# Performance work log

Measured on AMD Instinct MI355X. Metric: run time of the kernel, lower is better.

Reference implementation:

```python
import jax, jax.numpy as jnp
import numpy as np

HEADS = 4
TOKEN_DIM = 128
SCALE = (TOKEN_DIM // HEADS) ** -0.5


def _conv1x1(x, w, b):
    # x: (B,C,D,H,W), w: (O,C), b: (O,)
    return jnp.einsum('bcdhw,oc->bodhw', x, w) + b[None, :, None, None, None]


def _flatten(x):
    # (B,C,D,H,W) -> (B,L,C)
    B, C = x.shape[0], x.shape[1]
    return x.reshape(B, C, -1).transpose(0, 2, 1)


def _mha(q, k, v):
    # q: (B,Lq,D), k/v: (B,Lk,D)
    B, Lq, Dq = q.shape
    Lk = k.shape[1]
    hd = Dq // HEADS
    qh = q.reshape(B, Lq, HEADS, hd).transpose(0, 2, 1, 3)
    kh = k.reshape(B, Lk, HEADS, hd).transpose(0, 2, 1, 3)
    vh = v.reshape(B, Lk, HEADS, hd).transpose(0, 2, 1, 3)
    attn = jnp.einsum('bhqd,bhkd->bhqk', qh, kh) * SCALE
    attn = jax.nn.softmax(attn, axis=-1)
    out = jnp.einsum('bhqk,bhkd->bhqd', attn, vh)
    return out.transpose(0, 2, 1, 3).reshape(B, Lq, Dq)


def setup_inputs() -> dict:
    key = jax.random.key(0)
    ks = jax.random.split(key, 10)
    B, C, D, H, W = 2, 64, 16, 16, 16
    return {
        'feat_ct': jax.random.normal(ks[0], (B, C, D, H, W), jnp.float32),
        'feat_pet': jax.random.normal(ks[1], (B, C, D, H, W), jnp.float32),
        'wq': jax.random.normal(ks[2], (TOKEN_DIM, C), jnp.float32) * 0.05,
        'bq': jax.random.normal(ks[3], (TOKEN_DIM,), jnp.float32) * 0.05,
        'wk': jax.random.normal(ks[4], (TOKEN_DIM, C), jnp.float32) * 0.05,
        'bk': jax.random.normal(ks[5], (TOKEN_DIM,), jnp.float32) * 0.05,
        'wv': jax.random.normal(ks[6], (TOKEN_DIM, C), jnp.float32) * 0.05,
        'bv': jax.random.normal(ks[7], (TOKEN_DIM,), jnp.float32) * 0.05,
        'wo': jax.random.normal(ks[8], (C, TOKEN_DIM), jnp.float32) * 0.05,
        'bo': jax.random.normal(ks[9], (C,), jnp.float32) * 0.05,
    }


def reference(feat_ct, feat_pet, wq, bq, wk, bk, wv, bv, wo, bo):
    B, C, D, H, W = feat_ct.shape
    q_ct = _flatten(_conv1x1(feat_ct, wq, bq))
    k_ct = _flatten(_conv1x1(feat_ct, wk, bk))
    v_ct = _flatten(_conv1x1(feat_ct, wv, bv))
    q_pet = _flatten(_conv1x1(feat_pet, wq, bq))
    k_pet = _flatten(_conv1x1(feat_pet, wk, bk))
    v_pet = _flatten(_conv1x1(feat_pet, wv, bv))

    ct_attn = _mha(q_ct, k_pet, v_pet)
    pet_attn = _mha(q_pet, k_ct, v_ct)

    # Original torch code does view(B, token_dim, -1).permute(0,2,1) followed by
    # unflatten's permute(0,2,1) -> net effect is a raw reinterpretation of the
    # contiguous (B, L, token_dim) buffer as (B, token_dim, D, H, W): a reshape.
    fused_ct = ((ct_attn + q_ct) * 0.5).reshape(B, TOKEN_DIM, D, H, W)
    fused_ct = _conv1x1(fused_ct, wo, bo)  # dropout is identity (eval)
    fused_pet = ((pet_attn + q_pet) * 0.5).reshape(B, TOKEN_DIM, D, H, W)
    fused_pet = _conv1x1(fused_pet, wo, bo)

    return feat_ct + fused_ct, feat_pet + fused_pet
```

## Files before the change

kernel.cpp:

```cpp
#include <hip/hip_runtime.h>

typedef __bf16 bf16x8 __attribute__((ext_vector_type(8)));
typedef float f32x4 __attribute__((ext_vector_type(4)));
typedef float f32x16 __attribute__((ext_vector_type(16)));
typedef unsigned short u16x8 __attribute__((ext_vector_type(8)));
typedef unsigned int u32x4 __attribute__((ext_vector_type(4)));
typedef unsigned int u32x2 __attribute__((ext_vector_type(2)));

constexpr int C_ = 64, TD_ = 128, L_ = 4096, B_ = 2, H_ = 4, HD_ = 32;
constexpr float SCALE_LOG2E = 0.25504821365f;

#if __has_builtin(__builtin_amdgcn_exp2f)
#define EXP2F __builtin_amdgcn_exp2f
#else
#define EXP2F exp2f
#endif

static __device__ __forceinline__ unsigned short f2bf(float f) {
  unsigned u = __builtin_bit_cast(unsigned, f);
  u += 0x7fffu + ((u >> 16) & 1u);
  return (unsigned short)(u >> 16);
}
static __device__ __forceinline__ float bf2f(unsigned short h) {
  unsigned u = ((unsigned)h) << 16;
  return __builtin_bit_cast(float, u);
}
static __device__ __forceinline__ unsigned cvt_pk_bf16(float lo, float hi) {
  unsigned r;
  asm("v_cvt_pk_bf16_f32 %0, %1, %2" : "=v"(r) : "v"(lo), "v"(hi));
  return r;
}
static __device__ __forceinline__ void plane_swap(unsigned& a, unsigned& b) {
  asm("v_permlane32_swap_b32 %0, %1" : "+v"(a), "+v"(b));
}
static __device__ __forceinline__ float xhalf_add(float x) {
  float a = x, b = x;
  asm("v_permlane32_swap_b32 %0, %1" : "+v"(a), "+v"(b));
  return a + b;
}
static __device__ __forceinline__ int rowf(int r, int hi) {
  return (r & 3) + 8 * (r >> 2) + 4 * hi;
}
static __device__ __forceinline__ bf16x8 pack8(const float* v) {
  unsigned p0 = cvt_pk_bf16(v[0], v[1]);
  unsigned p1 = cvt_pk_bf16(v[2], v[3]);
  unsigned p2 = cvt_pk_bf16(v[4], v[5]);
  unsigned p3 = cvt_pk_bf16(v[6], v[7]);
  return __builtin_bit_cast(bf16x8, (u32x4){p0, p1, p2, p3});
}

__global__ __launch_bounds__(256) void proj_kernel(
    const float* __restrict__ fct, const float* __restrict__ fpet,
    const float* __restrict__ wq, const float* __restrict__ bq,
    const float* __restrict__ wk, const float* __restrict__ bk,
    const float* __restrict__ wv, const float* __restrict__ bv,
    unsigned short* __restrict__ Qbf, unsigned short* __restrict__ Kbf,
    unsigned short* __restrict__ Vt, float* __restrict__ QT)
{
  __shared__ __align__(16) unsigned short Tb[2][32][136];

  int bid = blockIdx.x;
  int lt = bid & 127, mb = bid >> 7;
  int l0 = lt * 32;
  int b = mb & 1;
  const float* xb = (mb >= 2 ? fpet : fct) + (size_t)b * C_ * L_;

  int lane = threadIdx.x & 63, wid = threadIdx.x >> 6;
  int l31 = lane & 31, hi = lane >> 5;
  int o0 = wid * 96;

  bf16x8 Bf[4];
  #pragma unroll
  for (int ch = 0; ch < 4; ++ch) {
    float v[8];
    #pragma unroll
    for (int j = 0; j < 8; ++j)
      v[j] = xb[(size_t)(ch * 16 + hi * 8 + j) * L_ + l0 + l31];
    Bf[ch] = pack8(v);
  }

  const f32x16 Z = {0.f, 0.f, 0.f, 0.f, 0.f, 0.f, 0.f, 0.f,
                    0.f, 0.f, 0.f, 0.f, 0.f, 0.f, 0.f, 0.f};
  f32x16 acc[3] = {Z, Z, Z};

  #pragma unroll
  for (int t = 0; t < 3; ++t) {
    int oa = o0 + t * 32;
    int which = oa >> 7, od = oa & 127;
    const float* W = which == 0 ? wq : (which == 1 ? wk : wv);
    #pragma unroll
    for (int ch = 0; ch < 4; ++ch) {
      const float* wr = W + (size_t)(od + l31) * C_ + ch * 16 + hi * 8;
      float a[8];
      #pragma unroll
      for (int j = 0; j < 8; ++j) a[j] = wr[j];
      bf16x8 Af = pack8(a);
      acc[t] = __builtin_amdgcn_mfma_f32_32x32x16_bf16(Af, Bf[ch], acc[t], 0, 0, 0);
    }
  }

  #pragma unroll
  for (int t = 0; t < 3; ++t) {
    int oa = o0 + t * 32;
    int which = oa >> 7, od = oa & 127;
    const float* Bs = which == 0 ? bq : (which == 1 ? bk : bv);
    if (which == 2) {
      #pragma unroll
      for (int r = 0; r < 16; ++r) {
        int o = od + rowf(r, hi);
        Vt[((size_t)mb * TD_ + o) * L_ + l0 + l31] = f2bf(acc[t][r] + Bs[o]);
      }
    } else {
      if (which == 0) {
        #pragma unroll
        for (int r = 0; r < 16; ++r) {
          int o = od + rowf(r, hi);
          QT[((size_t)mb * TD_ + o) * L_ + l0 + l31] = acc[t][r] + Bs[o];
        }
      }
      float sc = which == 0 ? SCALE_LOG2E : 1.0f;
      #pragma unroll
      for (int rg = 0; rg < 4; ++rg) {
        int cb = od + 8 * rg + 4 * hi;
        float y0 = (acc[t][rg * 4 + 0] + Bs[cb + 0]) * sc;
        float y1 = (acc[t][rg * 4 + 1] + Bs[cb + 1]) * sc;
        float y2 = (acc[t][rg * 4 + 2] + Bs[cb + 2]) * sc;
        float y3 = (acc[t][rg * 4 + 3] + Bs[cb + 3]) * sc;
        u32x2 pk = {cvt_pk_bf16(y0, y1), cvt_pk_bf16(y2, y3)};
        *(u32x2*)&Tb[which][l31][cb] = pk;
      }
    }
  }
  __syncthreads();

  int lrd = threadIdx.x & 31, sel = threadIdx.x >> 5;
  #pragma unroll
  for (int bufi = 0; bufi < 2; ++bufi) {
    unsigned short* dstg = bufi ? Kbf : Qbf;
    #pragma unroll
    for (int it = 0; it < 2; ++it) {
      int idx = it * 8 + sel;
      int h = idx >> 2, dc = idx & 3;
      u16x8 v = *(const u16x8*)&Tb[bufi][lrd][h * 32 + dc * 8];
      *(u16x8*)&dstg[(((size_t)mb * H_ + h) * L_ + l0 + lrd) * HD_ + dc * 8] = v;
    }
  }
}

static __device__ __forceinline__ void softmax_pv(
    const f32x16& S, float& lp, f32x16& O, bf16x8 vc0, bf16x8 vc1)
{
  float p[16];
  #pragma unroll
  for (int i = 0; i < 16; ++i) p[i] = EXP2F(S[i]);
  float s0 = (p[0] + p[1]) + (p[2] + p[3]);
  float s1 = (p[4] + p[5]) + (p[6] + p[7]);
  float s2 = (p[8] + p[9]) + (p[10] + p[11]);
  float s3 = (p[12] + p[13]) + (p[14] + p[15]);
  lp += (s0 + s1) + (s2 + s3);

  unsigned w0 = cvt_pk_bf16(p[0], p[1]);
  unsigned w1 = cvt_pk_bf16(p[2], p[3]);
  unsigned w2 = cvt_pk_bf16(p[4], p[5]);
  unsigned w3 = cvt_pk_bf16(p[6], p[7]);
  unsigned w4 = cvt_pk_bf16(p[8], p[9]);
  unsigned w5 = cvt_pk_bf16(p[10], p[11]);
  unsigned w6 = cvt_pk_bf16(p[12], p[13]);
  unsigned w7 = cvt_pk_bf16(p[14], p[15]);
  plane_swap(w0, w2);
  plane_swap(w1, w3);
  plane_swap(w4, w6);
  plane_swap(w5, w7);
  bf16x8 pf0 = __builtin_bit_cast(bf16x8, (u32x4){w0, w1, w2, w3});
  bf16x8 pf1 = __builtin_bit_cast(bf16x8, (u32x4){w4, w5, w6, w7});

  O = __builtin_amdgcn_mfma_f32_32x32x16_bf16(vc0, pf0, O, 0, 0, 0);
  O = __builtin_amdgcn_mfma_f32_32x32x16_bf16(vc1, pf1, O, 0, 0, 0);
}

__global__ __launch_bounds__(256, 4) void attn_kernel(
    const unsigned short* __restrict__ Qbf, const unsigned short* __restrict__ Kbf,
    const unsigned short* __restrict__ Vt, const float* __restrict__ QT,
    float* __restrict__ Fused)
{
  __shared__ __align__(16) float Obuf[4][64][33];
  __shared__ float lbuf[4][64];

  int bid = blockIdx.x;
  int x = bid & 7, local = bid >> 3;
  int g = 2 * x + (local & 1);
  int qg = local >> 1;
  int h = g & 3, b = (g >> 2) & 1, dir = g >> 3;

  int lane = threadIdx.x & 63, wid = threadIdx.x >> 6;
  int l31 = lane & 31, hi = lane >> 5;
  int q0 = qg * 64;
  int qmb = dir * B_ + b, kmb = (1 - dir) * B_ + b;
  int k0 = wid * 1024;

  const unsigned short* qbase = Qbf + (size_t)(qmb * H_ + h) * L_ * HD_;
  bf16x8 qb[2][2];
  #pragma unroll
  for (int s = 0; s < 2; ++s)
    #pragma unroll
    for (int c = 0; c < 2; ++c)
      qb[s][c] = *(const bf16x8*)(qbase + (q0 + s * 32 + l31) * HD_ + c * 16 + hi * 8);

  const unsigned short* kp =
      Kbf + (size_t)(kmb * H_ + h) * L_ * HD_ + (k0 + l31) * HD_ + hi * 8;
  const unsigned short* vp =
      Vt + (size_t)(kmb * TD_ + h * HD_ + l31) * L_ + k0 + hi * 8;

  const f32x16 Z = {0.f, 0.f, 0.f, 0.f, 0.f, 0.f, 0.f, 0.f,
                    0.f, 0.f, 0.f, 0.f, 0.f, 0.f, 0.f, 0.f};
  f32x16 Oa[2] = {Z, Z};
  float lp[2] = {0.f, 0.f};

  bf16x8 kc0 = *(const bf16x8*)(kp);
  bf16x8 kc1 = *(const bf16x8*)(kp + 16);
  bf16x8 vc0 = *(const bf16x8*)(vp);
  bf16x8 vc1 = *(const bf16x8*)(vp + 16);

  #pragma unroll 4
  for (int t = 0; t < 32; ++t) {
    bf16x8 kn0 = *(const bf16x8*)(kp + (t + 1) * 1024);
    bf16x8 kn1 = *(const bf16x8*)(kp + (t + 1) * 1024 + 16);
    bf16x8 vn0 = *(const bf16x8*)(vp + (t + 1) * 32);
    bf16x8 vn1 = *(const bf16x8*)(vp + (t + 1) * 32 + 16);
    #pragma unroll
    for (int s = 0; s < 2; ++s) {
      f32x16 S = __builtin_amdgcn_mfma_f32_32x32x16_bf16(kc0, qb[s][0], Z, 0, 0, 0);
      S = __builtin_amdgcn_mfma_f32_32x32x16_bf16(kc1, qb[s][1], S, 0, 0, 0);
      softmax_pv(S, lp[s], Oa[s], vc0, vc1);
    }
    kc0 = kn0; kc1 = kn1; vc0 = vn0; vc1 = vn1;
  }

  lp[0] = xhalf_add(lp[0]);
  lp[1] = xhalf_add(lp[1]);
  if (hi == 0) {
    lbuf[wid][l31] = lp[0];
    lbuf[wid][32 + l31] = lp[1];
  }
  #pragma unroll
  for (int r = 0; r < 16; ++r) {
    int d = rowf(r, hi);
    Obuf[wid][l31][d] = Oa[0][r];
    Obuf[wid][32 + l31][d] = Oa[1][r];
  }
  __syncthreads();

  float T = (lbuf[0][lane] + lbuf[1][lane]) + (lbuf[2][lane] + lbuf[3][lane]);
  float inv = 1.0f / T;
  const float* qtp = QT + ((size_t)qmb * TD_ + h * HD_) * L_ + q0 + lane;
  float vals[8];
  #pragma unroll
  for (int j = 0; j < 8; ++j) {
    int d = wid * 8 + j;
    float acc = (Obuf[0][lane][d] + Obuf[1][lane][d]) +
                (Obuf[2][lane][d] + Obuf[3][lane][d]);
    vals[j] = (acc * inv + qtp[(size_t)d * L_]) * 0.5f;
  }
  __syncthreads();
  #pragma unroll
  for (int j = 0; j < 8; ++j) Obuf[0][lane][wid * 8 + j] = vals[j];
  __syncthreads();
  int q = threadIdx.x >> 2, dq = threadIdx.x & 3;
  f32x4 u0 = *(const f32x4*)&Obuf[0][q][dq * 8];
  f32x4 u1 = *(const f32x4*)&Obuf[0][q][dq * 8 + 4];
  float* dst = Fused + ((size_t)qmb * L_ + q0 + q) * TD_ + h * HD_ + dq * 8;
  *(f32x4*)dst = u0;
  *(f32x4*)(dst + 4) = u1;
}

__global__ __launch_bounds__(256) void epi_kernel(
    const float* __restrict__ fct, const float* __restrict__ fpet,
    const float* __restrict__ wo, const float* __restrict__ bo,
    const float* __restrict__ Fused, float* __restrict__ out)
{
  __shared__ __align__(16) float red[2][32][33];

  int bid = blockIdx.x;
  int lt = bid & 127, im = bid >> 7;
  int b = im & 1, d = im >> 1;
  int l0 = lt * 32;
  int lr = l0 >> 7, col0 = l0 & 127;

  int lane = threadIdx.x & 63, wid = threadIdx.x >> 6;
  int l31 = lane & 31, hi = lane >> 5;
  int mt = wid & 1, kh = wid >> 1;
  int c0 = mt * 32;

  const float* Fb = Fused + (size_t)im * L_ * TD_;
  const f32x16 Z = {0.f, 0.f, 0.f, 0.f, 0.f, 0.f, 0.f, 0.f,
                    0.f, 0.f, 0.f, 0.f, 0.f, 0.f, 0.f, 0.f};
  f32x16 acc = Z;

  #pragma unroll
  for (int ch = 0; ch < 4; ++ch) {
    int cha = kh * 4 + ch;
    const float* wr = wo + (size_t)(c0 + l31) * TD_ + cha * 16 + hi * 8;
    float ah[8], al[8], vh[8], vl[8];
    #pragma unroll
    for (int j = 0; j < 8; ++j) {
      float v = wr[j];
      float hf = bf2f(f2bf(v));
      ah[j] = hf;
      al[j] = v - hf;
    }
    #pragma unroll
    for (int j = 0; j < 8; ++j) {
      int o = cha * 16 + hi * 8 + j;
      float v = Fb[(size_t)(o * 32 + lr) * TD_ + col0 + l31];
      float hf = bf2f(f2bf(v));
      vh[j] = hf;
      vl[j] = v - hf;
    }
    bf16x8 Ah = pack8(ah), Al = pack8(al);
    bf16x8 Bh = pack8(vh), Bl = pack8(vl);
    acc = __builtin_amdgcn_mfma_f32_32x32x16_bf16(Ah, Bh, acc, 0, 0, 0);
    acc = __builtin_amdgcn_mfma_f32_32x32x16_bf16(Ah, Bl, acc, 0, 0, 0);
    acc = __builtin_amdgcn_mfma_f32_32x32x16_bf16(Al, Bh, acc, 0, 0, 0);
  }

  if (kh == 1) {
    #pragma unroll
    for (int r = 0; r < 16; ++r) red[mt][rowf(r, hi)][l31] = acc[r];
  }
  __syncthreads();
  if (kh == 0) {
    const float* feat = (d ? fpet : fct) + (size_t)b * C_ * L_;
    float* ob = out + (size_t)im * C_ * L_;
    int l = l0 + l31;
    #pragma unroll
    for (int r = 0; r < 16; ++r) {
      int row = rowf(r, hi);
      int c = c0 + row;
      float v = acc[r] + red[mt][row][l31];
      ob[(size_t)c * L_ + l] = feat[(size_t)c * L_ + l] + bo[c] + v;
    }
  }
}

extern "C" void kernel_launch(void* const* d_in, const int* in_sizes, int n_in,
                              void* d_out, int out_size, void* d_ws, size_t ws_size,
                              hipStream_t stream)
{
  const float* fct  = (const float*)d_in[0];
  const float* fpet = (const float*)d_in[1];
  const float* wq = (const float*)d_in[2];
  const float* bq = (const float*)d_in[3];
  const float* wk = (const float*)d_in[4];
  const float* bk = (const float*)d_in[5];
  const float* wv = (const float*)d_in[6];
  const float* bv = (const float*)d_in[7];
  const float* wo = (const float*)d_in[8];
  const float* bo = (const float*)d_in[9];
  float* out = (float*)d_out;

  unsigned short* Qbf = (unsigned short*)d_ws;
  unsigned short* Kbf = Qbf + 2097152;
  unsigned short* Vt  = Kbf + 2097152;
  float* QT    = (float*)(Vt + 2097152);
  float* Fused = QT + 2097152;

  proj_kernel<<<512, 256, 0, stream>>>(fct, fpet, wq, bq, wk, bk, wv, bv,
                                       Qbf, Kbf, Vt, QT);
  attn_kernel<<<1024, 256, 0, stream>>>(Qbf, Kbf, Vt, QT, Fused);
  epi_kernel<<<512, 256, 0, stream>>>(fct, fpet, wo, bo, Fused, out);
}
```

Measured before the change: 158.1 us.

## Split projection grid by Q/K/V, store fused output as bf16 hi/lo pairs

The projection kernel now launches three times as many blocks, each computing one of Q, K or V for a 32-token tile, so each block does less work and more blocks run in parallel. The attention epilogue packs its partial outputs as fp16 in shared memory and writes the fused result as two bf16 planes (high and low) instead of fp32. The output kernel then loads those planes with vector reads, transposes them through shared memory, and feeds them straight to the split-precision MFMA without converting on the fly. The cross-wave reduction in fp16 and the bf16 hi+lo representation may lose a little precision, and the extra projection blocks reload the input features three times.

```diff
diff --git a/kernel.cpp b/kernel.cpp
--- a/kernel.cpp
+++ b/kernel.cpp
@@ -3,6 +3,7 @@
 typedef __bf16 bf16x8 __attribute__((ext_vector_type(8)));
 typedef float f32x4 __attribute__((ext_vector_type(4)));
 typedef float f32x16 __attribute__((ext_vector_type(16)));
+typedef _Float16 f16x2 __attribute__((ext_vector_type(2)));
 typedef unsigned short u16x8 __attribute__((ext_vector_type(8)));
 typedef unsigned int u32x4 __attribute__((ext_vector_type(4)));
 typedef unsigned int u32x2 __attribute__((ext_vector_type(2)));
@@ -29,6 +30,9 @@
   unsigned r;
   asm("v_cvt_pk_bf16_f32 %0, %1, %2" : "=v"(r) : "v"(lo), "v"(hi));
   return r;
+}
+static __device__ __forceinline__ unsigned cvt_pk_f16(float lo, float hi) {
+  return __builtin_bit_cast(unsigned, __builtin_amdgcn_cvt_pkrtz(lo, hi));
 }
 static __device__ __forceinline__ void plane_swap(unsigned& a, unsigned& b) {
   asm("v_permlane32_swap_b32 %0, %1" : "+v"(a), "+v"(b));
@@ -57,93 +61,73 @@
     unsigned short* __restrict__ Qbf, unsigned short* __restrict__ Kbf,
     unsigned short* __restrict__ Vt, float* __restrict__ QT)
 {
-  __shared__ __align__(16) unsigned short Tb[2][32][136];
+  __shared__ __align__(16) unsigned short Tb[32][136];
 
   int bid = blockIdx.x;
-  int lt = bid & 127, mb = bid >> 7;
+  int lt = bid & 127;
+  int rest = bid >> 7;
+  int mb = rest & 3;
+  int which = rest >> 2;
   int l0 = lt * 32;
   int b = mb & 1;
   const float* xb = (mb >= 2 ? fpet : fct) + (size_t)b * C_ * L_;
 
   int lane = threadIdx.x & 63, wid = threadIdx.x >> 6;
   int l31 = lane & 31, hi = lane >> 5;
-  int o0 = wid * 96;
-
-  bf16x8 Bf[4];
+  int od = wid * 32;
+
+  const float* W  = which == 0 ? wq : (which == 1 ? wk : wv);
+  const float* Bs = which == 0 ? bq : (which == 1 ? bk : bv);
+
+  const f32x16 Z = {0.f, 0.f, 0.f, 0.f, 0.f, 0.f, 0.f, 0.f,
+                    0.f, 0.f, 0.f, 0.f, 0.f, 0.f, 0.f, 0.f};
+  f32x16 acc = Z;
   #pragma unroll
   for (int ch = 0; ch < 4; ++ch) {
-    float v[8];
+    float v[8], a[8];
     #pragma unroll
     for (int j = 0; j < 8; ++j)
       v[j] = xb[(size_t)(ch * 16 + hi * 8 + j) * L_ + l0 + l31];
-    Bf[ch] = pack8(v);
-  }
-
-  const f32x16 Z = {0.f, 0.f, 0.f, 0.f, 0.f, 0.f, 0.f, 0.f,
-                    0.f, 0.f, 0.f, 0.f, 0.f, 0.f, 0.f, 0.f};
-  f32x16 acc[3] = {Z, Z, Z};
-
-  #pragma unroll
-  for (int t = 0; t < 3; ++t) {
-    int oa = o0 + t * 32;
-    int which = oa >> 7, od = oa & 127;
-    const float* W = which == 0 ? wq : (which == 1 ? wk : wv);
-    #pragma unroll
-    for (int ch = 0; ch < 4; ++ch) {
-      const float* wr = W + (size_t)(od + l31) * C_ + ch * 16 + hi * 8;
-      float a[8];
-      #pragma unroll
-      for (int j = 0; j < 8; ++j) a[j] = wr[j];
-      bf16x8 Af = pack8(a);
-      acc[t] = __builtin_amdgcn_mfma_f32_32x32x16_bf16(Af, Bf[ch], acc[t], 0, 0, 0);
-    }
-  }
-
-  #pragma unroll
-  for (int t = 0; t < 3; ++t) {
-    int oa = o0 + t * 32;
-    int which = oa >> 7, od = oa & 127;
-    const float* Bs = which == 0 ? bq : (which == 1 ? bk : bv);
-    if (which == 2) {
+    const float* wr = W + (size_t)(od + l31) * C_ + ch * 16 + hi * 8;
+    #pragma unroll
+    for (int j = 0; j < 8; ++j) a[j] = wr[j];
+    acc = __builtin_amdgcn_mfma_f32_32x32x16_bf16(pack8(a), pack8(v), acc, 0, 0, 0);
+  }
+
+  if (which == 2) {
+    #pragma unroll
+    for (int r = 0; r < 16; ++r) {
+      int o = od + rowf(r, hi);
+      Vt[((size_t)mb * TD_ + o) * L_ + l0 + l31] = f2bf(acc[r] + Bs[o]);
+    }
+  } else {
+    if (which == 0) {
       #pragma unroll
       for (int r = 0; r < 16; ++r) {
         int o = od + rowf(r, hi);
-        Vt[((size_t)mb * TD_ + o) * L_ + l0 + l31] = f2bf(acc[t][r] + Bs[o]);
+        QT[((size_t)mb * TD_ + o) * L_ + l0 + l31] = acc[r] + Bs[o];
       }
-    } else {
-      if (which == 0) {
-        #pragma unroll
-        for (int r = 0; r < 16; ++r) {
-          int o = od + rowf(r, hi);
-          QT[((size_t)mb * TD_ + o) * L_ + l0 + l31] = acc[t][r] + Bs[o];
-        }
-      }
-      float sc = which == 0 ? SCALE_LOG2E : 1.0f;
-      #pragma unroll
-      for (int rg = 0; rg < 4; ++rg) {
-        int cb = od + 8 * rg + 4 * hi;
-        float y0 = (acc[t][rg * 4 + 0] + Bs[cb + 0]) * sc;
-        float y1 = (acc[t][rg * 4 + 1] + Bs[cb + 1]) * sc;
-        float y2 = (acc[t][rg * 4 + 2] + Bs[cb + 2]) * sc;
-        float y3 = (acc[t][rg * 4 + 3] + Bs[cb + 3]) * sc;
-        u32x2 pk = {cvt_pk_bf16(y0, y1), cvt_pk_bf16(y2, y3)};
-        *(u32x2*)&Tb[which][l31][cb] = pk;
-      }
-    }
-  }
-  __syncthreads();
-
-  int lrd = threadIdx.x & 31, sel = threadIdx.x >> 5;
-  #pragma unroll
-  for (int bufi = 0; bufi < 2; ++bufi) {
-    unsigned short* dstg = bufi ? Kbf : Qbf;
-    #pragma unroll
-    for (int it = 0; it < 2; ++it) {
-      int idx = it * 8 + sel;
-      int h = idx >> 2, dc = idx & 3;
-      u16x8 v = *(const u16x8*)&Tb[bufi][lrd][h * 32 + dc * 8];
-      *(u16x8*)&dstg[(((size_t)mb * H_ + h) * L_ + l0 + lrd) * HD_ + dc * 8] = v;
-    }
+    }
+    float sc = which == 0 ? SCALE_LOG2E : 1.0f;
+    #pragma unroll
+    for (int rg = 0; rg < 4; ++rg) {
+      int cb = od + 8 * rg + 4 * hi;
+      float y0 = (acc[rg * 4 + 0] + Bs[cb + 0]) * sc;
+      float y1 = (acc[rg * 4 + 1] + Bs[cb + 1]) * sc;
+      float y2 = (acc[rg * 4 + 2] + Bs[cb + 2]) * sc;
+      float y3 = (acc[rg * 4 + 3] + Bs[cb + 3]) * sc;
+      u32x2 pk = {cvt_pk_bf16(y0, y1), cvt_pk_bf16(y2, y3)};
+      *(u32x2*)&Tb[l31][cb] = pk;
+    }
+    __syncthreads();
+    unsigned short* dstg = which ? Kbf : Qbf;
+    int row = threadIdx.x >> 3, chunk = threadIdx.x & 7;
+    int h = chunk >> 1, d0 = (chunk & 1) * 16;
+    u16x8 v0 = *(const u16x8*)&Tb[row][chunk * 16];
+    u16x8 v1 = *(const u16x8*)&Tb[row][chunk * 16 + 8];
+    size_t gb = (((size_t)mb * H_ + h) * L_ + l0 + row) * HD_ + d0;
+    *(u16x8*)&dstg[gb] = v0;
+    *(u16x8*)&dstg[gb + 8] = v1;
   }
 }
 
@@ -181,9 +165,9 @@
 __global__ __launch_bounds__(256, 4) void attn_kernel(
     const unsigned short* __restrict__ Qbf, const unsigned short* __restrict__ Kbf,
     const unsigned short* __restrict__ Vt, const float* __restrict__ QT,
-    float* __restrict__ Fused)
-{
-  __shared__ __align__(16) float Obuf[4][64][33];
+    unsigned short* __restrict__ Fh, unsigned short* __restrict__ Fl)
+{
+  __shared__ __align__(16) unsigned Obuf[4][64][17];
   __shared__ float lbuf[4][64];
 
   int bid = blockIdx.x;
@@ -243,11 +227,13 @@
     lbuf[wid][32 + l31] = lp[1];
   }
   #pragma unroll
-  for (int r = 0; r < 16; ++r) {
-    int d = rowf(r, hi);
-    Obuf[wid][l31][d] = Oa[0][r];
-    Obuf[wid][32 + l31][d] = Oa[1][r];
-  }
+  for (int s = 0; s < 2; ++s)
+    #pragma unroll
+    for (int r = 0; r < 16; r += 2) {
+      unsigned pk2 = cvt_pk_f16(Oa[s][r], Oa[s][r + 1]);
+      int d2 = ((r & 3) >> 1) + 4 * (r >> 2) + 2 * hi;
+      Obuf[wid][s * 32 + l31][d2] = pk2;
+    }
   __syncthreads();
 
   float T = (lbuf[0][lane] + lbuf[1][lane]) + (lbuf[2][lane] + lbuf[3][lane]);
@@ -255,29 +241,44 @@
   const float* qtp = QT + ((size_t)qmb * TD_ + h * HD_) * L_ + q0 + lane;
   float vals[8];
   #pragma unroll
-  for (int j = 0; j < 8; ++j) {
-    int d = wid * 8 + j;
-    float acc = (Obuf[0][lane][d] + Obuf[1][lane][d]) +
-                (Obuf[2][lane][d] + Obuf[3][lane][d]);
-    vals[j] = (acc * inv + qtp[(size_t)d * L_]) * 0.5f;
-  }
-  __syncthreads();
-  #pragma unroll
-  for (int j = 0; j < 8; ++j) Obuf[0][lane][wid * 8 + j] = vals[j];
+  for (int jp = 0; jp < 4; ++jp) {
+    float se = 0.f, so = 0.f;
+    #pragma unroll
+    for (int w = 0; w < 4; ++w) {
+      f16x2 v = __builtin_bit_cast(f16x2, Obuf[w][lane][wid * 4 + jp]);
+      se += (float)v[0];
+      so += (float)v[1];
+    }
+    int dd = wid * 8 + jp * 2;
+    vals[jp * 2]     = (se * inv + qtp[(size_t)dd * L_]) * 0.5f;
+    vals[jp * 2 + 1] = (so * inv + qtp[(size_t)(dd + 1) * L_]) * 0.5f;
+  }
+  __syncthreads();
+
+  unsigned (*Sb)[64][17] = (unsigned (*)[64][17])Obuf;
+  #pragma unroll
+  for (int jp = 0; jp < 4; ++jp) {
+    float v0 = vals[jp * 2], v1 = vals[jp * 2 + 1];
+    float h0 = bf2f(f2bf(v0)), h1 = bf2f(f2bf(v1));
+    Sb[0][lane][wid * 4 + jp] = cvt_pk_bf16(v0, v1);
+    Sb[1][lane][wid * 4 + jp] = cvt_pk_bf16(v0 - h0, v1 - h1);
+  }
   __syncthreads();
   int q = threadIdx.x >> 2, dq = threadIdx.x & 3;
-  f32x4 u0 = *(const f32x4*)&Obuf[0][q][dq * 8];
-  f32x4 u1 = *(const f32x4*)&Obuf[0][q][dq * 8 + 4];
-  float* dst = Fused + ((size_t)qmb * L_ + q0 + q) * TD_ + h * HD_ + dq * 8;
-  *(f32x4*)dst = u0;
-  *(f32x4*)(dst + 4) = u1;
+  u32x4 vh = *(const u32x4*)&Sb[0][q][dq * 4];
+  u32x4 vl = *(const u32x4*)&Sb[1][q][dq * 4];
+  size_t gb = ((size_t)qmb * L_ + q0 + q) * TD_ + h * HD_ + dq * 8;
+  *(u16x8*)&Fh[gb] = __builtin_bit_cast(u16x8, vh);
+  *(u16x8*)&Fl[gb] = __builtin_bit_cast(u16x8, vl);
 }
 
 __global__ __launch_bounds__(256) void epi_kernel(
     const float* __restrict__ fct, const float* __restrict__ fpet,
     const float* __restrict__ wo, const float* __restrict__ bo,
-    const float* __restrict__ Fused, float* __restrict__ out)
-{
+    const unsigned short* __restrict__ Fh, const unsigned short* __restrict__ Fl,
+    float* __restrict__ out)
+{
+  __shared__ __align__(16) unsigned short Gh[32][136], Gl[32][136];
   __shared__ __align__(16) float red[2][32][33];
 
   int bid = blockIdx.x;
@@ -286,21 +287,17 @@
   int l0 = lt * 32;
   int lr = l0 >> 7, col0 = l0 & 127;
 
-  int lane = threadIdx.x & 63, wid = threadIdx.x >> 6;
+  int tid = threadIdx.x;
+  int lane = tid & 63, wid = tid >> 6;
   int l31 = lane & 31, hi = lane >> 5;
   int mt = wid & 1, kh = wid >> 1;
   int c0 = mt * 32;
 
-  const float* Fb = Fused + (size_t)im * L_ * TD_;
-  const f32x16 Z = {0.f, 0.f, 0.f, 0.f, 0.f, 0.f, 0.f, 0.f,
-                    0.f, 0.f, 0.f, 0.f, 0.f, 0.f, 0.f, 0.f};
-  f32x16 acc = Z;
-
+  bf16x8 Ah[4], Al[4];
   #pragma unroll
   for (int ch = 0; ch < 4; ++ch) {
-    int cha = kh * 4 + ch;
-    const float* wr = wo + (size_t)(c0 + l31) * TD_ + cha * 16 + hi * 8;
-    float ah[8], al[8], vh[8], vl[8];
+    const float* wr = wo + (size_t)(c0 + l31) * TD_ + (kh * 4 + ch) * 16 + hi * 8;
+    float ah[8], al[8];
     #pragma unroll
     for (int j = 0; j < 8; ++j) {
       float v = wr[j];
@@ -308,19 +305,41 @@
       ah[j] = hf;
       al[j] = v - hf;
     }
+    Ah[ch] = pack8(ah);
+    Al[ch] = pack8(al);
+  }
+
+  {
+    int o = tid & 127, half = tid >> 7;
+    size_t src = ((size_t)im * L_ + o * 32 + lr) * TD_ + col0 + half * 16;
+    u16x8 ha = *(const u16x8*)&Fh[src];
+    u16x8 hb = *(const u16x8*)&Fh[src + 8];
+    u16x8 la = *(const u16x8*)&Fl[src];
+    u16x8 lb = *(const u16x8*)&Fl[src + 8];
     #pragma unroll
     for (int j = 0; j < 8; ++j) {
-      int o = cha * 16 + hi * 8 + j;
-      float v = Fb[(size_t)(o * 32 + lr) * TD_ + col0 + l31];
-      float hf = bf2f(f2bf(v));
-      vh[j] = hf;
-      vl[j] = v - hf;
-    }
-    bf16x8 Ah = pack8(ah), Al = pack8(al);
-    bf16x8 Bh = pack8(vh), Bl = pack8(vl);
-    acc = __builtin_amdgcn_mfma_f32_32x32x16_bf16(Ah, Bh, acc, 0, 0, 0);
-    acc = __builtin_amdgcn_mfma_f32_32x32x16_bf16(Ah, Bl, acc, 0, 0, 0);
-    acc = __builtin_amdgcn_mfma_f32_32x32x16_bf16(Al, Bh, acc, 0, 0, 0);
+      Gh[half * 16 + j][o] = ha[j];
+      Gl[half * 16 + j][o] = la[j];
+    }
+    #pragma unroll
+    for (int j = 0; j < 8; ++j) {
+      Gh[half * 16 + 8 + j][o] = hb[j];
+      Gl[half * 16 + 8 + j][o] = lb[j];
+    }
+  }
+  __syncthreads();
+
+  const f32x16 Z = {0.f, 0.f, 0.f, 0.f, 0.f, 0.f, 0.f, 0.f,
+                    0.f, 0.f, 0.f, 0.f, 0.f, 0.f, 0.f, 0.f};
+  f32x16 acc = Z;
+  #pragma unroll
+  for (int ch = 0; ch < 4; ++ch) {
+    int ko = (kh * 4 + ch) * 16 + hi * 8;
+    bf16x8 Bh = *(const bf16x8*)&Gh[l31][ko];
+    bf16x8 Bl = *(const bf16x8*)&Gl[l31][ko];
+    acc = __builtin_amdgcn_mfma_f32_32x32x16_bf16(Ah[ch], Bh, acc, 0, 0, 0);
+    acc = __builtin_amdgcn_mfma_f32_32x32x16_bf16(Ah[ch], Bl, acc, 0, 0, 0);
+    acc = __builtin_amdgcn_mfma_f32_32x32x16_bf16(Al[ch], Bh, acc, 0, 0, 0);
   }
 
   if (kh == 1) {
@@ -361,11 +380,12 @@
   unsigned short* Qbf = (unsigned short*)d_ws;
   unsigned short* Kbf = Qbf + 2097152;
   unsigned short* Vt  = Kbf + 2097152;
-  float* QT    = (float*)(Vt + 2097152);
-  float* Fused = QT + 2097152;
-
-  proj_kernel<<<512, 256, 0, stream>>>(fct, fpet, wq, bq, wk, bk, wv, bv,
-                                       Qbf, Kbf, Vt, QT);
-  attn_kernel<<<1024, 256, 0, stream>>>(Qbf, Kbf, Vt, QT, Fused);
-  epi_kernel<<<512, 256, 0, stream>>>(fct, fpet, wo, bo, Fused, out);
-}
+  float* QT = (float*)(Vt + 2097152);
+  unsigned short* Fh = (unsigned short*)(QT + 2097152);
+  unsigned short* Fl = Fh + 2097152;
+
+  proj_kernel<<<1536, 256, 0, stream>>>(fct, fpet, wq, bq, wk, bk, wv, bv,
+                                        Qbf, Kbf, Vt, QT);
+  attn_kernel<<<1024, 256, 0, stream>>>(Qbf, Kbf, Vt, QT, Fh, Fl);
+  epi_kernel<<<512, 256, 0, stream>>>(fct, fpet, wo, bo, Fh, Fl, out);
+}
```

Result: faster. 146.2 us (-7.5%).
